# Kernel optimization log

Measured on AMD Instinct MI355X. Metric: run time of the kernel, lower is better.

The kernel has to match this reference:

```python
import jax, jax.numpy as jnp
import numpy as np

B, L, H, S = 16, 2048, 1024, 32
P, N_ASP, N_RAT = 256, 8, 5


def _layernorm(x, scale, bias, eps=1e-5):
    mu = jnp.mean(x, axis=-1, keepdims=True)
    var = jnp.mean(jnp.square(x - mu), axis=-1, keepdims=True)
    return (x - mu) * jax.lax.rsqrt(var + eps) * scale + bias


def _bndl(x, ln_s, ln_b, W):
    # BnDropLin eval: LayerNorm -> (Dropout off) -> Linear(no bias)
    return _layernorm(x, ln_s, ln_b) @ W


def setup_inputs() -> dict:
    key = jax.random.key(0)
    ks = jax.random.split(key, 8)
    outputs = jax.random.normal(ks[0], (B, L, H), dtype=jnp.float32)
    mask = jnp.ones((B, L), dtype=jnp.float32)
    # p_index: binary sentence-boundary markers, exactly S per doc, min gap 2
    rng = np.random.default_rng(0)
    p = np.zeros((B, L), dtype=np.int32)
    for b in range(B):
        idx = np.sort(rng.choice(L // 2 - 1, size=S, replace=False)) * 2 + 1
        p[b, idx] = 1
    p_index = jnp.asarray(p)
    sc = 0.02
    params = dict(
        ln_a_s=jnp.ones((H,), jnp.float32), ln_a_b=jnp.zeros((H,), jnp.float32),
        W_a=jax.random.normal(ks[1], (H, P), jnp.float32) * sc,
        ln_s_s=jnp.ones((H,), jnp.float32), ln_s_b=jnp.zeros((H,), jnp.float32),
        W_s=jax.random.normal(ks[2], (H, P), jnp.float32) * sc,
        ln_asp_s=jnp.ones((P,), jnp.float32), ln_asp_b=jnp.zeros((P,), jnp.float32),
        W_asp=jax.random.normal(ks[3], (P, N_ASP + 1), jnp.float32) * sc,
        ln_se_s=jnp.ones((P,), jnp.float32), ln_se_b=jnp.zeros((P,), jnp.float32),
        W_se=jax.random.normal(ks[4], (P, N_RAT), jnp.float32) * sc,
    )
    return dict(outputs=outputs, mask=mask, p_index=p_index, n_sent=S, **params)


def _segment_means(proj, end, start):
    # proj: [B, L, P]; start/end: [B, S] token index ranges [start, end)
    c = jnp.concatenate([jnp.zeros_like(proj[:, :1]), jnp.cumsum(proj, axis=1)], axis=1)  # [B,L+1,P]
    s_end = jnp.take_along_axis(c, end[:, :, None], axis=1)
    s_beg = jnp.take_along_axis(c, start[:, :, None], axis=1)
    cnt = (end - start).astype(proj.dtype)[:, :, None]
    return (s_end - s_beg) / cnt  # [B, S, P]


def reference(outputs, mask, p_index, n_sent,
              ln_a_s, ln_a_b, W_a, ln_s_s, ln_s_b, W_s,
              ln_asp_s, ln_asp_b, W_asp, ln_se_s, ln_se_b, W_se):
    b, l, h = outputs.shape
    n_asp = W_asp.shape[1] - 1
    flat = outputs.reshape(-1, h)
    a_proj = jax.nn.gelu(_bndl(flat, ln_a_s, ln_a_b, W_a), approximate=False).reshape(b, l, -1)
    s_proj = jax.nn.gelu(_bndl(flat, ln_s_s, ln_s_b, W_s), approximate=False).reshape(b, l, -1)
    # sentence boundaries: positions of nonzeros (exactly n_sent per row)
    pos = jnp.where(p_index > 0, jnp.arange(l)[None, :], l)
    pi = jnp.sort(pos, axis=1)[:, :n_sent]                      # [B,S] boundary idx (exclusive end)
    start = jnp.concatenate([jnp.zeros_like(pi[:, :1]), pi[:, :-1] + 1], axis=1)
    a_sent = _segment_means(a_proj, pi, start)                  # [B,S,P]
    s_sent = _segment_means(s_proj, pi, start)                  # [B,S,P]
    a_flat = a_sent.reshape(b * n_sent, -1)
    s_flat = s_sent.reshape(b * n_sent, -1)
    aspect_dist = jax.nn.softmax(_bndl(a_flat, ln_asp_s, ln_asp_b, W_asp), axis=1)  # [N, n_asp+1]
    aw = aspect_dist[:, :n_asp]                                 # [N, n_asp]
    sent_bmm = aw[:, :, None] * s_flat[:, None, :]              # [N, n_asp, P]
    doc_sum = sent_bmm.reshape(b, n_sent, n_asp, -1).sum(axis=1)        # [B, n_asp, P]
    w_sum = aw.reshape(b, n_sent, n_asp).sum(axis=1)[:, :, None]        # [B, n_asp, 1]
    doc_emb = doc_sum / w_sum
    # shared sentiment head (ModuleList([m]*n_asp) aliases one module)
    result = _bndl(doc_emb, ln_se_s, ln_se_b, W_se)             # [B, n_asp, n_rat]
    aspect_doc = aspect_dist.reshape(b, n_sent, n_asp + 1)
    return (result, outputs, aspect_doc)
```

## Files before the change

### kernel.cpp

```cpp
#include <hip/hip_runtime.h>
#include <cstdint>
#include <cstddef>

#define B_   16
#define L_   2048
#define H_   1024
#define S_   32
#define P_   256
#define NASP 8
#define NRAT 5
#define M_   (B_*L_)
#define N_   (2*P_)

typedef unsigned short u16;
typedef __bf16 bf16;
typedef u16  u16x4  __attribute__((ext_vector_type(4)));
typedef u16  u16x8  __attribute__((ext_vector_type(8)));
typedef bf16 bf16x8 __attribute__((ext_vector_type(8)));
typedef float f32x4 __attribute__((ext_vector_type(4)));

__device__ __forceinline__ u16 f2b(float f){
  unsigned int u = __float_as_uint(f);
  u += 0x7FFFu + ((u >> 16) & 1u);
  return (u16)(u >> 16);
}
__device__ __forceinline__ float b2f(u16 v){
  return __uint_as_float(((unsigned int)v) << 16);
}

__device__ __forceinline__ void gload_lds16(const u16* g, u16* l){
  __builtin_amdgcn_global_load_lds(
      (const __attribute__((address_space(1))) unsigned int*)g,
      (__attribute__((address_space(3))) unsigned int*)l, 16, 0, 0);
}

__device__ __forceinline__ float2 block_reduce2(float a, float b){
  __shared__ float sh[8];
  #pragma unroll
  for (int o = 32; o > 0; o >>= 1){
    a += __shfl_down(a, o, 64);
    b += __shfl_down(b, o, 64);
  }
  int w = threadIdx.x >> 6;
  if ((threadIdx.x & 63) == 0){ sh[w] = a; sh[w + 4] = b; }
  __syncthreads();
  float2 r;
  r.x = sh[0] + sh[1] + sh[2] + sh[3];
  r.y = sh[4] + sh[5] + sh[6] + sh[7];
  __syncthreads();
  return r;
}

__global__ void fold_k(const float* __restrict__ Wa, const float* __restrict__ Ws,
                       const float* __restrict__ sa, const float* __restrict__ ba,
                       const float* __restrict__ ss, const float* __restrict__ bs,
                       u16* __restrict__ WcT, float* __restrict__ biasc){
  int n = blockIdx.x;
  const float* W; const float* sc; const float* bi; int col;
  if (n < P_){ W = Wa; sc = sa; bi = ba; col = n; }
  else       { W = Ws; sc = ss; bi = bs; col = n - P_; }
  float bacc = 0.f;
  #pragma unroll
  for (int i = 0; i < 4; ++i){
    int k = threadIdx.x + i * 256;
    float w = W[(size_t)k * P_ + col];
    WcT[(size_t)n * H_ + k] = f2b(w * sc[k]);
    bacc += w * bi[k];
  }
  float2 r = block_reduce2(bacc, 0.f);
  if (threadIdx.x == 0) biasc[n] = r.x;
}

__global__ void markers_k(const int* __restrict__ p_index, int* __restrict__ pi){
  int b = blockIdx.x;
  int lane = threadIdx.x;
  int cnt = 0;
  for (int c = 0; c < L_ / 64; ++c){
    int pos = c * 64 + lane;
    bool f = p_index[(size_t)b * L_ + pos] > 0;
    unsigned long long m = __ballot(f);
    int before = __popcll(m & ((1ull << lane) - 1ull));
    if (f){
      int idx = cnt + before;
      if (idx < S_) pi[b * S_ + idx] = pos;
    }
    cnt += __popcll(m);
  }
}

template<bool FUSE_ECHO>
__global__ void stats_xhat_k(const float* __restrict__ x, u16* __restrict__ xhat,
                             float4* __restrict__ echo){
  int row = blockIdx.x;
  int t = threadIdx.x;
  float4 v = ((const float4*)(x + (size_t)row * H_))[t];
  if (FUSE_ECHO) echo[(size_t)row * (H_ / 4) + t] = v;
  float s  = v.x + v.y + v.z + v.w;
  float ss = v.x*v.x + v.y*v.y + v.z*v.z + v.w*v.w;
  float2 r = block_reduce2(s, ss);
  float mean = r.x * (1.f / H_);
  float var  = fmaxf(r.y * (1.f / H_) - mean * mean, 0.f);
  float rstd = rsqrtf(var + 1e-5f);
  u16x4 o;
  o[0] = f2b((v.x - mean) * rstd);
  o[1] = f2b((v.y - mean) * rstd);
  o[2] = f2b((v.z - mean) * rstd);
  o[3] = f2b((v.w - mean) * rstd);
  ((u16x4*)(xhat + (size_t)row * H_))[t] = o;
}

__global__ __launch_bounds__(512, 2) void gemm_k(const u16* __restrict__ xhat,
                                                 const u16* __restrict__ WcT,
                                                 const float* __restrict__ biasc,
                                                 u16* __restrict__ proj){
  __shared__ __align__(16) u16 As[256 * 64];
  __shared__ __align__(16) u16 Bs[256 * 64];
  int t = threadIdx.x;
  unsigned int l = blockIdx.x;
  unsigned int xcd  = l & 7;
  unsigned int slot = l >> 3;
  int nbase = (int)(slot & 1) * 256;
  int mbase = (int)(xcd * 16 + (slot >> 1)) * 256;

  int w = t >> 6, lane = t & 63;
  int wr = w >> 2, wc = w & 3;
  int quad = lane >> 4, l15 = lane & 15;

  int rin = lane >> 3;
  int g = (lane & 7) ^ rin;
  const u16* gA[4]; const u16* gB[4]; u16* lA[4]; u16* lB[4];
  #pragma unroll
  for (int i = 0; i < 4; ++i){
    int r = w * 32 + i * 8 + rin;
    gA[i] = xhat + (size_t)(mbase + r) * H_ + g * 8;
    gB[i] = WcT  + (size_t)(nbase + r) * H_ + g * 8;
    lA[i] = As + (w * 4 + i) * 512;
    lB[i] = Bs + (w * 4 + i) * 512;
  }

  f32x4 acc[8][4] = {};

  for (int kk = 0; kk < H_; kk += 64){
    __syncthreads();
    #pragma unroll
    for (int i = 0; i < 4; ++i){
      gload_lds16(gA[i] + kk, lA[i]);
      gload_lds16(gB[i] + kk, lB[i]);
    }
    __syncthreads();

    #pragma unroll
    for (int s = 0; s < 2; ++s){
      bf16x8 af[8], bfr[4];
      #pragma unroll
      for (int im = 0; im < 8; ++im){
        int R = wr * 128 + im * 16 + l15;
        int c = (s * 4 + quad) ^ (R & 7);
        af[im] = *reinterpret_cast<const bf16x8*>(&As[R * 64 + c * 8]);
      }
      #pragma unroll
      for (int in = 0; in < 4; ++in){
        int R = wc * 64 + in * 16 + l15;
        int c = (s * 4 + quad) ^ (R & 7);
        bfr[in] = *reinterpret_cast<const bf16x8*>(&Bs[R * 64 + c * 8]);
      }
      #pragma unroll
      for (int im = 0; im < 8; ++im)
        #pragma unroll
        for (int in = 0; in < 4; ++in)
          acc[im][in] = __builtin_amdgcn_mfma_f32_16x16x32_bf16(af[im], bfr[in], acc[im][in], 0, 0, 0);
    }
  }

  #pragma unroll
  for (int in = 0; in < 4; ++in){
    int col = nbase + wc * 64 + in * 16 + l15;
    float bv = biasc[col];
    #pragma unroll
    for (int im = 0; im < 8; ++im){
      #pragma unroll
      for (int r = 0; r < 4; ++r){
        int rowg = mbase + wr * 128 + im * 16 + quad * 4 + r;
        float vv = acc[im][in][r] + bv;
        float gl = 0.5f * vv * (1.0f + erff(vv * 0.70710678118654752f));
        proj[(size_t)rowg * N_ + col] = f2b(gl);
      }
    }
  }
}

__global__ __launch_bounds__(1024) void segmean_k(const u16* __restrict__ proj,
                                                  const int* __restrict__ pi,
                                                  float* __restrict__ sent){
  int b = blockIdx.x, j = blockIdx.y;
  int t = threadIdx.x;
  int rg   = t >> 6;
  int lane = t & 63;
  int end   = pi[b * S_ + j];
  int start = (j == 0) ? 0 : (pi[b * S_ + j - 1] + 1);
  end   = min(max(end, 0), L_);
  start = min(max(start, 0), end);
  int cnt = max(end - start, 1);
  float inv = 1.0f / (float)cnt;

  float s[8] = {};
  const u16* base = proj + ((size_t)b * L_ + start) * N_ + lane * 8;
  for (int r = rg; r < cnt; r += 16){
    u16x8 v = *reinterpret_cast<const u16x8*>(base + (size_t)r * N_);
    #pragma unroll
    for (int k = 0; k < 8; ++k) s[k] += b2f(v[k]);
  }

  __shared__ float sh[16][N_];
  #pragma unroll
  for (int k = 0; k < 8; ++k) sh[rg][lane * 8 + k] = s[k];
  __syncthreads();

  if (t < N_){
    float acc = 0.f;
    #pragma unroll
    for (int g = 0; g < 16; ++g) acc += sh[g][t];
    sent[((size_t)b * S_ + j) * N_ + t] = acc * inv;
  }
}

__global__ void aspect_k(const float* __restrict__ sent,
                         const float* __restrict__ lns, const float* __restrict__ lnb,
                         const float* __restrict__ Wasp,
                         float* __restrict__ out_adoc, float* __restrict__ aw){
  int sidx = blockIdx.x;
  int t = threadIdx.x;
  float a = sent[(size_t)sidx * N_ + t];
  float2 r = block_reduce2(a, a * a);
  float mean = r.x * (1.f / P_);
  float var  = fmaxf(r.y * (1.f / P_) - mean * mean, 0.f);
  float rstd = rsqrtf(var + 1e-5f);
  __shared__ float shv[P_];
  shv[t] = (a - mean) * rstd * lns[t] + lnb[t];
  __syncthreads();
  __shared__ float lg[NASP + 1];
  if (t < NASP + 1){
    float acc = 0.f;
    for (int p = 0; p < P_; ++p) acc += shv[p] * Wasp[p * (NASP + 1) + t];
    lg[t] = acc;
  }
  __syncthreads();
  __shared__ float pr[NASP + 1];
  if (t == 0){
    float m = lg[0];
    #pragma unroll
    for (int i = 1; i < NASP + 1; ++i) m = fmaxf(m, lg[i]);
    float s = 0.f;
    #pragma unroll
    for (int i = 0; i < NASP + 1; ++i){ float e = expf(lg[i] - m); pr[i] = e; s += e; }
    float is = 1.f / s;
    #pragma unroll
    for (int i = 0; i < NASP + 1; ++i) pr[i] *= is;
  }
  __syncthreads();
  if (t < NASP + 1) out_adoc[(size_t)sidx * (NASP + 1) + t] = pr[t];
  if (t < NASP)     aw[(size_t)sidx * NASP + t] = pr[t];
}

__global__ void result_k(const float* __restrict__ sent, const float* __restrict__ aw,
                         const float* __restrict__ lns, const float* __restrict__ lnb,
                         const float* __restrict__ Wse, float* __restrict__ out){
  int ba = blockIdx.x;
  int b = ba >> 3, a = ba & 7;
  int t = threadIdx.x;
  float acc = 0.f, wsum = 0.f;
  for (int s2 = 0; s2 < S_; ++s2){
    float w = aw[((size_t)(b * S_ + s2)) * NASP + a];
    acc  += w * sent[((size_t)(b * S_ + s2)) * N_ + P_ + t];
    wsum += w;
  }
  float d = acc / fmaxf(wsum, 1e-20f);
  float2 r = block_reduce2(d, d * d);
  float mean = r.x * (1.f / P_);
  float var  = fmaxf(r.y * (1.f / P_) - mean * mean, 0.f);
  float rstd = rsqrtf(var + 1e-5f);
  __shared__ float shv[P_];
  shv[t] = (d - mean) * rstd * lns[t] + lnb[t];
  __syncthreads();
  if (t < NRAT){
    float s = 0.f;
    for (int p = 0; p < P_; ++p) s += shv[p] * Wse[p * NRAT + t];
    out[(size_t)ba * NRAT + t] = s;
  }
}

__global__ void copy_k(const float4* __restrict__ src, float4* __restrict__ dst){
  size_t i = (size_t)blockIdx.x * 256 + threadIdx.x;
  dst[i] = src[i];
}

extern "C" void kernel_launch(void* const* d_in, const int* in_sizes, int n_in,
                              void* d_out, int out_size, void* d_ws, size_t ws_size,
                              hipStream_t stream) {
  const float* x        = (const float*)d_in[0];
  const int*   p_index  = (const int*)d_in[2];
  const float* ln_a_s   = (const float*)d_in[4];
  const float* ln_a_b   = (const float*)d_in[5];
  const float* W_a      = (const float*)d_in[6];
  const float* ln_s_s   = (const float*)d_in[7];
  const float* ln_s_b   = (const float*)d_in[8];
  const float* W_s      = (const float*)d_in[9];
  const float* ln_asp_s = (const float*)d_in[10];
  const float* ln_asp_b = (const float*)d_in[11];
  const float* W_asp    = (const float*)d_in[12];
  const float* ln_se_s  = (const float*)d_in[13];
  const float* ln_se_b  = (const float*)d_in[14];
  const float* W_se     = (const float*)d_in[15];

  float* out_result = (float*)d_out;
  float* out_echo   = out_result + 640;
  float* out_adoc   = out_echo + (size_t)M_ * H_;

  char* ws = (char*)d_ws;
  u16*   WcT   = (u16*)ws;   ws += (size_t)N_ * H_ * 2;
  float* biasc = (float*)ws; ws += (size_t)N_ * 4;
  int*   pi    = (int*)ws;   ws += (size_t)B_ * S_ * 4;
  float* sent  = (float*)ws; ws += (size_t)B_ * S_ * N_ * 4;
  float* aw    = (float*)ws; ws += (size_t)B_ * S_ * NASP * 4;

  size_t small_used = (size_t)(ws - (char*)d_ws);
  size_t big_need   = small_used + (size_t)M_ * N_ * 2 + (size_t)M_ * H_ * 2;
  bool   big_ws     = ws_size >= big_need;

  u16* proj; u16* xhat;
  if (big_ws){
    proj = (u16*)ws;
    xhat = proj + (size_t)M_ * N_;
  } else {
    proj = (u16*)out_echo;
    xhat = proj + (size_t)M_ * N_;
  }

  fold_k<<<N_, 256, 0, stream>>>(W_a, W_s, ln_a_s, ln_a_b, ln_s_s, ln_s_b, WcT, biasc);
  markers_k<<<B_, 64, 0, stream>>>(p_index, pi);
  if (big_ws)
    stats_xhat_k<true ><<<M_, 256, 0, stream>>>(x, xhat, (float4*)out_echo);
  else
    stats_xhat_k<false><<<M_, 256, 0, stream>>>(x, xhat, nullptr);
  gemm_k<<<256, 512, 0, stream>>>(xhat, WcT, biasc, proj);
  segmean_k<<<dim3(B_, S_), 1024, 0, stream>>>(proj, pi, sent);
  aspect_k<<<B_ * S_, 256, 0, stream>>>(sent, ln_asp_s, ln_asp_b, W_asp, out_adoc, aw);
  result_k<<<B_ * NASP, 256, 0, stream>>>(sent, aw, ln_se_s, ln_se_b, W_se, out_result);
  if (!big_ws)
    copy_k<<<(M_ * H_ / 4) / 256, 256, 0, stream>>>((const float4*)x, (float4*)out_echo);
}
```

Measured before the change: 399.6 us.

## Double-buffer LDS tiles in GEMM to overlap global loads with MFMA

The GEMM kernel now keeps two LDS buffers for the A and B tiles. It prefetches two K-tiles up front and, each iteration, issues the load for tile kt+2 into the buffer it just finished reading, using explicit vmcnt waits and raw s_barriers instead of two __syncthreads per tile. The aim is to hide global-to-LDS load latency behind MFMA work, with wave priority raised during the compute phase. LDS use doubles to 128KB per block, so two blocks can no longer share a CU. Since the grid is 256 blocks, likely about one per CU, this costs little.

```diff
diff --git a/kernel.cpp b/kernel.cpp
--- a/kernel.cpp
+++ b/kernel.cpp
@@ -109,12 +109,13 @@
   ((u16x4*)(xhat + (size_t)row * H_))[t] = o;
 }
 
+#define NT_ 16
 __global__ __launch_bounds__(512, 2) void gemm_k(const u16* __restrict__ xhat,
                                                  const u16* __restrict__ WcT,
                                                  const float* __restrict__ biasc,
                                                  u16* __restrict__ proj){
-  __shared__ __align__(16) u16 As[256 * 64];
-  __shared__ __align__(16) u16 Bs[256 * 64];
+  __shared__ __align__(16) u16 As[2][256 * 64];
+  __shared__ __align__(16) u16 Bs[2][256 * 64];
   int t = threadIdx.x;
   unsigned int l = blockIdx.x;
   unsigned int xcd  = l & 7;
@@ -128,27 +129,37 @@
 
   int rin = lane >> 3;
   int g = (lane & 7) ^ rin;
-  const u16* gA[4]; const u16* gB[4]; u16* lA[4]; u16* lB[4];
+  const u16* gA[4]; const u16* gB[4]; int off[4];
   #pragma unroll
   for (int i = 0; i < 4; ++i){
     int r = w * 32 + i * 8 + rin;
     gA[i] = xhat + (size_t)(mbase + r) * H_ + g * 8;
     gB[i] = WcT  + (size_t)(nbase + r) * H_ + g * 8;
-    lA[i] = As + (w * 4 + i) * 512;
-    lB[i] = Bs + (w * 4 + i) * 512;
+    off[i] = (w * 4 + i) * 512;
   }
 
   f32x4 acc[8][4] = {};
 
-  for (int kk = 0; kk < H_; kk += 64){
-    __syncthreads();
-    #pragma unroll
-    for (int i = 0; i < 4; ++i){
-      gload_lds16(gA[i] + kk, lA[i]);
-      gload_lds16(gB[i] + kk, lB[i]);
-    }
-    __syncthreads();
-
+#define STAGE_(buf, tile) do{ int kk_ = (tile) * 64;            \
+    gload_lds16(gA[0] + kk_, &As[buf][off[0]]);                 \
+    gload_lds16(gA[1] + kk_, &As[buf][off[1]]);                 \
+    gload_lds16(gA[2] + kk_, &As[buf][off[2]]);                 \
+    gload_lds16(gA[3] + kk_, &As[buf][off[3]]);                 \
+    gload_lds16(gB[0] + kk_, &Bs[buf][off[0]]);                 \
+    gload_lds16(gB[1] + kk_, &Bs[buf][off[1]]);                 \
+    gload_lds16(gB[2] + kk_, &Bs[buf][off[2]]);                 \
+    gload_lds16(gB[3] + kk_, &Bs[buf][off[3]]);                 \
+  }while(0)
+
+  STAGE_(0, 0);
+  STAGE_(1, 1);
+  asm volatile("s_waitcnt vmcnt(8)" ::: "memory");
+  __builtin_amdgcn_sched_barrier(0);
+  __builtin_amdgcn_s_barrier();
+
+  for (int kt = 0; kt < NT_; ++kt){
+    int cur = kt & 1;
+    __builtin_amdgcn_s_setprio(1);
     #pragma unroll
     for (int s = 0; s < 2; ++s){
       bf16x8 af[8], bfr[4];
@@ -156,13 +167,13 @@
       for (int im = 0; im < 8; ++im){
         int R = wr * 128 + im * 16 + l15;
         int c = (s * 4 + quad) ^ (R & 7);
-        af[im] = *reinterpret_cast<const bf16x8*>(&As[R * 64 + c * 8]);
+        af[im] = *reinterpret_cast<const bf16x8*>(&As[cur][R * 64 + c * 8]);
       }
       #pragma unroll
       for (int in = 0; in < 4; ++in){
         int R = wc * 64 + in * 16 + l15;
         int c = (s * 4 + quad) ^ (R & 7);
-        bfr[in] = *reinterpret_cast<const bf16x8*>(&Bs[R * 64 + c * 8]);
+        bfr[in] = *reinterpret_cast<const bf16x8*>(&Bs[cur][R * 64 + c * 8]);
       }
       #pragma unroll
       for (int im = 0; im < 8; ++im)
@@ -170,7 +181,19 @@
         for (int in = 0; in < 4; ++in)
           acc[im][in] = __builtin_amdgcn_mfma_f32_16x16x32_bf16(af[im], bfr[in], acc[im][in], 0, 0, 0);
     }
-  }
+    __builtin_amdgcn_s_setprio(0);
+    if (kt == NT_ - 1) break;
+    __builtin_amdgcn_s_barrier();
+    if (kt + 2 < NT_){
+      STAGE_(cur, kt + 2);
+      asm volatile("s_waitcnt vmcnt(8)" ::: "memory");
+    } else {
+      asm volatile("s_waitcnt vmcnt(0)" ::: "memory");
+    }
+    __builtin_amdgcn_sched_barrier(0);
+    __builtin_amdgcn_s_barrier();
+  }
+#undef STAGE_
 
   #pragma unroll
   for (int in = 0; in < 4; ++in){
```

New measurement: 393.5 us. Within noise of the previous version (-1.5%).
